# Performance work log

Hardware: AMD Instinct MI355X
Metric: run time of the kernel (lower is better)

The kernel has to match this reference:

```python
import jax, jax.numpy as jnp
import numpy as np

POOL = 7  # pool_size (7x7)


def setup_inputs() -> dict:
    key = jax.random.key(0)
    kb, kw, k2, k3, k4, k5 = jax.random.split(key, 6)
    B, N, C = 2, 1000, 256
    # boxes: (y1, x1, y2, x2) normalized, guaranteed y1<y2, x1<x2, inside [0,1]
    yx = jax.random.uniform(kb, (B, N, 2), dtype=jnp.float32)
    wh = jax.random.uniform(kw, (B, N, 2), dtype=jnp.float32) * 0.3 + 0.01
    y1x1 = yx * (1.0 - wh)
    y2x2 = y1x1 + wh
    boxes = jnp.concatenate([y1x1, y2x2], axis=-1)
    image_shape = jnp.array([1024, 1024, 3], dtype=jnp.int32)
    feat2 = jax.random.normal(k2, (B, 256, 256, C), dtype=jnp.float32)
    feat3 = jax.random.normal(k3, (B, 128, 128, C), dtype=jnp.float32)
    feat4 = jax.random.normal(k4, (B, 64, 64, C), dtype=jnp.float32)
    feat5 = jax.random.normal(k5, (B, 32, 32, C), dtype=jnp.float32)
    return dict(boxes=boxes, image_shape=image_shape,
                feat2=feat2, feat3=feat3, feat4=feat4, feat5=feat5)


def _crop_and_resize(feat, boxes, box_idx, P):
    """TF tf.image.crop_and_resize semantics (bilinear, extrapolation_value=0).

    feat: [B, H, W, C]; boxes: [M, 4] normalized; box_idx: [M] int32.
    Returns [M, P, P, C].
    """
    H, W = feat.shape[1], feat.shape[2]
    y1, x1, y2, x2 = (boxes[:, 0], boxes[:, 1], boxes[:, 2], boxes[:, 3])
    i = jnp.arange(P, dtype=feat.dtype)
    # sample coordinates in source-pixel space (P > 1 branch of TF kernel)
    ys = y1[:, None] * (H - 1) + i[None, :] * ((y2 - y1) * (H - 1) / (P - 1))[:, None]  # [M,P]
    xs = x1[:, None] * (W - 1) + i[None, :] * ((x2 - x1) * (W - 1) / (P - 1))[:, None]  # [M,P]

    def corners(s, L):
        s0 = jnp.floor(s)
        frac = s - s0
        i0 = jnp.clip(s0.astype(jnp.int32), 0, L - 1)
        i1 = jnp.clip(i0 + 1, 0, L - 1)
        valid = (s >= 0) & (s <= L - 1)
        return i0, i1, frac, valid

    y0, y1i, fy, vy = corners(ys, H)
    x0, x1i, fx, vx = corners(xs, W)
    b = box_idx[:, None, None]
    # 4 bilinear corners, each gathered as [M, P, P, C]
    v00 = feat[b, y0[:, :, None], x0[:, None, :]]
    v01 = feat[b, y0[:, :, None], x1i[:, None, :]]
    v10 = feat[b, y1i[:, :, None], x0[:, None, :]]
    v11 = feat[b, y1i[:, :, None], x1i[:, None, :]]
    fy_ = fy[:, :, None, None]
    fx_ = fx[:, None, :, None]
    top = v00 * (1 - fx_) + v01 * fx_
    bot = v10 * (1 - fx_) + v11 * fx_
    out = top * (1 - fy_) + bot * fy_
    mask = (vy[:, :, None] & vx[:, None, :])[..., None]
    return jnp.where(mask, out, jnp.zeros((), feat.dtype))


def reference(boxes, image_shape, feat2, feat3, feat4, feat5):
    B, N = boxes.shape[0], boxes.shape[1]
    P = POOL
    boxes_flat = boxes.reshape(B * N, 4)
    box_idx = jnp.repeat(jnp.arange(B, dtype=jnp.int32), N)
    h = boxes_flat[:, 2] - boxes_flat[:, 0]
    w = boxes_flat[:, 3] - boxes_flat[:, 1]
    area = (image_shape[0] * image_shape[1]).astype(jnp.float32)
    # FPN level routing: level = clip(4 + round(log2(sqrt(wh)*sqrt(area)/224)), 2, 5)
    lvl = jnp.log(jnp.sqrt(w * h) * jnp.sqrt(area) / 224.0) / jnp.log(2.0)
    lvl = jnp.clip(4.0 + jnp.round(lvl), 2.0, 5.0).astype(jnp.int32)
    feats = (feat2, feat3, feat4, feat5)
    C = feat2.shape[-1]
    out = jnp.zeros((B * N, P, P, C), dtype=feat2.dtype)
    for i, level in enumerate((2, 3, 4, 5)):
        crop = _crop_and_resize(feats[i], boxes_flat, box_idx, P)
        sel = (lvl == level)[:, None, None, None]
        out = jnp.where(sel, crop, out)
    # original sorts by 100000*batch + box_id to restore order; our dense
    # select already produces the original (batch, box) ordering.
    return out.reshape(B, N, P, P, C)
```

## Files before the change

kernel.cpp:

```cpp
#include <hip/hip_runtime.h>

#define POOL 7
#define CCH  256

typedef float f32x4 __attribute__((ext_vector_type(4)));

__global__ __launch_bounds__(256) void roialign_rows(
    const float* __restrict__ boxes,
    const int*   __restrict__ image_shape,
    const float* __restrict__ feat2,
    const float* __restrict__ feat3,
    const float* __restrict__ feat4,
    const float* __restrict__ feat5,
    float*       __restrict__ out,
    int N, int total_rows)
{
    const int P = POOL;
    const int wave = threadIdx.x >> 6;
    const int lane = threadIdx.x & 63;
    const int task = blockIdx.x * 4 + wave;
    if (task >= total_rows) return;

    const int m  = task / P;
    const int py = task - m * P;
    const int b  = m / N;

    const float y1 = boxes[m * 4 + 0];
    const float x1 = boxes[m * 4 + 1];
    const float y2 = boxes[m * 4 + 2];
    const float x2 = boxes[m * 4 + 3];
    const float h  = y2 - y1;
    const float w  = x2 - x1;
    const float area = (float)(image_shape[0] * image_shape[1]);

    const float lvlf = logf(sqrtf(w * h) * sqrtf(area) / 224.0f) * 1.4426950408889634f;
    const int lvl = (int)fminf(fmaxf(4.0f + rintf(lvlf), 2.0f), 5.0f);

    const float* feat;
    int H;
    switch (lvl) {
        case 2:  feat = feat2; H = 256; break;
        case 3:  feat = feat3; H = 128; break;
        case 4:  feat = feat4; H = 64;  break;
        default: feat = feat5; H = 32;  break;
    }
    const int W = H;

    const float sy = y1 * (float)(H - 1) + (float)py * (h * (float)(H - 1) / (float)(P - 1));
    const float y0f = floorf(sy);
    const float fy  = sy - y0f;
    int yi0 = (int)y0f;
    yi0 = yi0 < 0 ? 0 : (yi0 > H - 1 ? H - 1 : yi0);
    const int yi1 = yi0 + 1 > H - 1 ? H - 1 : yi0 + 1;
    const bool vy = (sy >= 0.0f) && (sy <= (float)(H - 1));

    const int c = lane * 4;

    const float* __restrict__ fb   = feat + (size_t)b * ((size_t)H * W * CCH);
    const float* __restrict__ row0 = fb + (size_t)yi0 * W * CCH + c;
    const float* __restrict__ row1 = fb + (size_t)yi1 * W * CCH + c;
    float* __restrict__ orow = out + ((size_t)m * (P * P) + (size_t)py * P) * CCH + c;

    const float xbase = x1 * (float)(W - 1);
    const float xstep = w * (float)(W - 1) / (float)(P - 1);
    const float gy = 1.0f - fy;

#pragma unroll
    for (int px = 0; px < P; ++px) {
        const float sx  = xbase + (float)px * xstep;
        const float x0f = floorf(sx);
        const float fx  = sx - x0f;
        int xi0 = (int)x0f;
        xi0 = xi0 < 0 ? 0 : (xi0 > W - 1 ? W - 1 : xi0);
        const int xi1 = xi0 + 1 > W - 1 ? W - 1 : xi0 + 1;
        const bool valid = vy && (sx >= 0.0f) && (sx <= (float)(W - 1));

        const f32x4 v00 = *(const f32x4*)(row0 + xi0 * CCH);
        const f32x4 v01 = *(const f32x4*)(row0 + xi1 * CCH);
        const f32x4 v10 = *(const f32x4*)(row1 + xi0 * CCH);
        const f32x4 v11 = *(const f32x4*)(row1 + xi1 * CCH);

        const float gx = 1.0f - fx;
        f32x4 r = (v00 * gx + v01 * fx) * gy + (v10 * gx + v11 * fx) * fy;
        const float vm = valid ? 1.0f : 0.0f;
        r *= vm;

        __builtin_nontemporal_store(r, (f32x4*)(orow + px * CCH));
    }
}

extern "C" void kernel_launch(void* const* d_in, const int* in_sizes, int n_in,
                              void* d_out, int out_size, void* d_ws, size_t ws_size,
                              hipStream_t stream) {
    const float* boxes       = (const float*)d_in[0];
    const int*   image_shape = (const int*)  d_in[1];
    const float* feat2       = (const float*)d_in[2];
    const float* feat3       = (const float*)d_in[3];
    const float* feat4       = (const float*)d_in[4];
    const float* feat5       = (const float*)d_in[5];
    float*       out         = (float*)d_out;

    const int B = 2;
    const int N = in_sizes[0] / (B * 4);
    const int total_rows = B * N * POOL;

    const int rows_per_block = 4;
    const int grid = (total_rows + rows_per_block - 1) / rows_per_block;

    roialign_rows<<<grid, 256, 0, stream>>>(
        boxes, image_shape, feat2, feat3, feat4, feat5, out,
        N, total_rows);
}
```

Measured before the change: 255.6 us.

## Bucket boxes by FPN level and process one box per block

Adds a pre-pass that computes each box's pyramid level and appends it to a per-level list with atomics. The main kernel then gives each block one box, grouped by level, and loops its waves over the pooled rows. The goal is to group work by feature map so the cache gets better locality and waves in a block diverge less. In exchange it adds two extra kernel launches. It also leaves 3 of 4 waves with uneven work, since 7 rows are spread over 4 waves.

```diff
diff --git a/kernel.cpp b/kernel.cpp
--- a/kernel.cpp
+++ b/kernel.cpp
@@ -5,25 +5,65 @@
 
 typedef float f32x4 __attribute__((ext_vector_type(4)));
 
-__global__ __launch_bounds__(256) void roialign_rows(
+__global__ void zero_counters(int* __restrict__ cnt) {
+    if (threadIdx.x < 4) cnt[threadIdx.x] = 0;
+}
+
+__global__ void bucket_boxes(const float* __restrict__ boxes,
+                             const int*   __restrict__ image_shape,
+                             int M,
+                             int* __restrict__ cnt,
+                             int* __restrict__ lists)
+{
+    const int m = blockIdx.x * blockDim.x + threadIdx.x;
+    if (m >= M) return;
+    const float y1 = boxes[m * 4 + 0];
+    const float x1 = boxes[m * 4 + 1];
+    const float y2 = boxes[m * 4 + 2];
+    const float x2 = boxes[m * 4 + 3];
+    const float h  = y2 - y1;
+    const float w  = x2 - x1;
+    const float area = (float)(image_shape[0] * image_shape[1]);
+    const float lvlf = logf(sqrtf(w * h) * sqrtf(area) / 224.0f) * 1.4426950408889634f;
+    const int lvl = (int)fminf(fmaxf(4.0f + rintf(lvlf), 2.0f), 5.0f);
+    const int l = lvl - 2;
+    const int idx = atomicAdd(&cnt[l], 1);
+    lists[l * M + idx] = m;
+    (void)x1;
+}
+
+__global__ __launch_bounds__(256) void roialign_boxes(
     const float* __restrict__ boxes,
-    const int*   __restrict__ image_shape,
     const float* __restrict__ feat2,
     const float* __restrict__ feat3,
     const float* __restrict__ feat4,
     const float* __restrict__ feat5,
+    const int*   __restrict__ cnt,
+    const int*   __restrict__ lists,
     float*       __restrict__ out,
-    int N, int total_rows)
+    int M, int N)
 {
     const int P = POOL;
-    const int wave = threadIdx.x >> 6;
-    const int lane = threadIdx.x & 63;
-    const int task = blockIdx.x * 4 + wave;
-    if (task >= total_rows) return;
+    const int j = blockIdx.x;
 
-    const int m  = task / P;
-    const int py = task - m * P;
-    const int b  = m / N;
+    const int c0 = cnt[0], c1 = cnt[1], c2 = cnt[2];
+    int l, r = j;
+    if (j < c0)               { l = 0; }
+    else if (j < c0 + c1)     { l = 1; r = j - c0; }
+    else if (j < c0 + c1 + c2){ l = 2; r = j - c0 - c1; }
+    else                      { l = 3; r = j - c0 - c1 - c2; }
+    const int m = lists[l * M + r];
+    const int b = m / N;
+
+    const float* feat;
+    switch (l) {
+        case 0:  feat = feat2; break;
+        case 1:  feat = feat3; break;
+        case 2:  feat = feat4; break;
+        default: feat = feat5; break;
+    }
+    const int H = 256 >> l;
+    const int W = H;
 
     const float y1 = boxes[m * 4 + 0];
     const float x1 = boxes[m * 4 + 1];
@@ -31,61 +71,54 @@
     const float x2 = boxes[m * 4 + 3];
     const float h  = y2 - y1;
     const float w  = x2 - x1;
-    const float area = (float)(image_shape[0] * image_shape[1]);
 
-    const float lvlf = logf(sqrtf(w * h) * sqrtf(area) / 224.0f) * 1.4426950408889634f;
-    const int lvl = (int)fminf(fmaxf(4.0f + rintf(lvlf), 2.0f), 5.0f);
+    const int wave = threadIdx.x >> 6;
+    const int lane = threadIdx.x & 63;
+    const int c    = lane * 4;
 
-    const float* feat;
-    int H;
-    switch (lvl) {
-        case 2:  feat = feat2; H = 256; break;
-        case 3:  feat = feat3; H = 128; break;
-        case 4:  feat = feat4; H = 64;  break;
-        default: feat = feat5; H = 32;  break;
-    }
-    const int W = H;
+    const float* __restrict__ fb = feat + (size_t)b * ((size_t)H * W * CCH);
+    float* __restrict__ obox = out + (size_t)m * (P * P) * CCH + c;
 
-    const float sy = y1 * (float)(H - 1) + (float)py * (h * (float)(H - 1) / (float)(P - 1));
-    const float y0f = floorf(sy);
-    const float fy  = sy - y0f;
-    int yi0 = (int)y0f;
-    yi0 = yi0 < 0 ? 0 : (yi0 > H - 1 ? H - 1 : yi0);
-    const int yi1 = yi0 + 1 > H - 1 ? H - 1 : yi0 + 1;
-    const bool vy = (sy >= 0.0f) && (sy <= (float)(H - 1));
-
-    const int c = lane * 4;
-
-    const float* __restrict__ fb   = feat + (size_t)b * ((size_t)H * W * CCH);
-    const float* __restrict__ row0 = fb + (size_t)yi0 * W * CCH + c;
-    const float* __restrict__ row1 = fb + (size_t)yi1 * W * CCH + c;
-    float* __restrict__ orow = out + ((size_t)m * (P * P) + (size_t)py * P) * CCH + c;
-
+    const float ybase = y1 * (float)(H - 1);
+    const float ystep = h * (float)(H - 1) / (float)(P - 1);
     const float xbase = x1 * (float)(W - 1);
     const float xstep = w * (float)(W - 1) / (float)(P - 1);
-    const float gy = 1.0f - fy;
+
+    for (int py = wave; py < P; py += 4) {
+        const float sy  = ybase + (float)py * ystep;
+        const float y0f = floorf(sy);
+        const float fy  = sy - y0f;
+        int yi0 = (int)y0f;
+        yi0 = yi0 < 0 ? 0 : (yi0 > H - 1 ? H - 1 : yi0);
+        const int yi1 = yi0 + 1 > H - 1 ? H - 1 : yi0 + 1;
+        const bool vy = (sy >= 0.0f) && (sy <= (float)(H - 1));
+        const float gy = 1.0f - fy;
+
+        const float* __restrict__ row0 = fb + (size_t)yi0 * W * CCH + c;
+        const float* __restrict__ row1 = fb + (size_t)yi1 * W * CCH + c;
+        float* __restrict__ orow = obox + (size_t)py * P * CCH;
 
 #pragma unroll
-    for (int px = 0; px < P; ++px) {
-        const float sx  = xbase + (float)px * xstep;
-        const float x0f = floorf(sx);
-        const float fx  = sx - x0f;
-        int xi0 = (int)x0f;
-        xi0 = xi0 < 0 ? 0 : (xi0 > W - 1 ? W - 1 : xi0);
-        const int xi1 = xi0 + 1 > W - 1 ? W - 1 : xi0 + 1;
-        const bool valid = vy && (sx >= 0.0f) && (sx <= (float)(W - 1));
+        for (int px = 0; px < P; ++px) {
+            const float sx  = xbase + (float)px * xstep;
+            const float x0f = floorf(sx);
+            const float fx  = sx - x0f;
+            int xi0 = (int)x0f;
+            xi0 = xi0 < 0 ? 0 : (xi0 > W - 1 ? W - 1 : xi0);
+            const int xi1 = xi0 + 1 > W - 1 ? W - 1 : xi0 + 1;
+            const bool valid = vy && (sx >= 0.0f) && (sx <= (float)(W - 1));
 
-        const f32x4 v00 = *(const f32x4*)(row0 + xi0 * CCH);
-        const f32x4 v01 = *(const f32x4*)(row0 + xi1 * CCH);
-        const f32x4 v10 = *(const f32x4*)(row1 + xi0 * CCH);
-        const f32x4 v11 = *(const f32x4*)(row1 + xi1 * CCH);
+            const f32x4 v00 = *(const f32x4*)(row0 + xi0 * CCH);
+            const f32x4 v01 = *(const f32x4*)(row0 + xi1 * CCH);
+            const f32x4 v10 = *(const f32x4*)(row1 + xi0 * CCH);
+            const f32x4 v11 = *(const f32x4*)(row1 + xi1 * CCH);
 
-        const float gx = 1.0f - fx;
-        f32x4 r = (v00 * gx + v01 * fx) * gy + (v10 * gx + v11 * fx) * fy;
-        const float vm = valid ? 1.0f : 0.0f;
-        r *= vm;
+            const float gx = 1.0f - fx;
+            f32x4 rv = (v00 * gx + v01 * fx) * gy + (v10 * gx + v11 * fx) * fy;
+            rv *= (valid ? 1.0f : 0.0f);
 
-        __builtin_nontemporal_store(r, (f32x4*)(orow + px * CCH));
+            __builtin_nontemporal_store(rv, (f32x4*)(orow + px * CCH));
+        }
     }
 }
 
@@ -102,12 +135,13 @@
 
     const int B = 2;
     const int N = in_sizes[0] / (B * 4);
-    const int total_rows = B * N * POOL;
+    const int M = B * N;
 
-    const int rows_per_block = 4;
-    const int grid = (total_rows + rows_per_block - 1) / rows_per_block;
+    int* cnt   = (int*)d_ws;
+    int* lists = (int*)d_ws + 8;
 
-    roialign_rows<<<grid, 256, 0, stream>>>(
-        boxes, image_shape, feat2, feat3, feat4, feat5, out,
-        N, total_rows);
+    zero_counters<<<1, 64, 0, stream>>>(cnt);
+    bucket_boxes<<<(M + 255) / 256, 256, 0, stream>>>(boxes, image_shape, M, cnt, lists);
+    roialign_boxes<<<M, 256, 0, stream>>>(boxes, feat2, feat3, feat4, feat5,
+                                          cnt, lists, out, M, N);
 }
```

After: 279.0 us. 9.1% more time.
